# Kernel tuning notes

Measured on AMD Instinct MI355X. Metric: run time of the kernel, lower is better.

The kernel has to match this reference:

```python
import jax, jax.numpy as jnp
import numpy as np

N_NODES = 50000
N_EDGES = 800000
IN_FEAT = 64
HIDDEN = 32
GRID = 4
OUT = 1
N_GRAPHS = 128
N_CONV = 2  # num_layers - 1
NEG_SLOPE = 0.01  # torch LeakyReLU default


def kan_apply(x, W, bias=None):
    # x: (B, in), W: (2, out, in, grid) -> (B, out)
    g = W.shape[-1]
    k = jnp.arange(1, g + 1, dtype=x.dtype)          # (grid,)
    arg = x[:, :, None] * k                           # (B, in, grid)
    y = (jnp.einsum('big,oig->bo', jnp.cos(arg), W[0])
         + jnp.einsum('big,oig->bo', jnp.sin(arg), W[1]))
    if bias is not None:
        y = y + bias
    return y


def setup_inputs() -> dict:
    key = jax.random.key(0)
    ks = jax.random.split(key, 8)
    x = jax.random.normal(ks[0], (N_NODES, IN_FEAT), dtype=jnp.float32)
    edge_index = jax.random.randint(ks[1], (2, N_EDGES), 0, N_NODES, dtype=jnp.int64)
    batch = jnp.sort(jax.random.randint(ks[2], (N_NODES,), 0, N_GRAPHS, dtype=jnp.int64))
    W_in = jax.random.normal(ks[3], (2, HIDDEN, IN_FEAT, GRID), dtype=jnp.float32) / np.float32(np.sqrt(IN_FEAT) * np.sqrt(GRID))
    W_conv = jax.random.normal(ks[4], (N_CONV, 2, HIDDEN, HIDDEN, GRID), dtype=jnp.float32) / np.float32(np.sqrt(HIDDEN) * np.sqrt(GRID))
    W_out = jax.random.normal(ks[5], (2, OUT, HIDDEN, 1), dtype=jnp.float32) / np.float32(np.sqrt(HIDDEN) * 1.0)
    b_out = jnp.zeros((1, OUT), dtype=jnp.float32)
    return {"x": x, "edge_index": edge_index, "batch": batch,
            "W_in": W_in, "W_conv": W_conv, "W_out": W_out, "b_out": b_out}


def reference(x, edge_index, batch, W_in, W_conv, W_out, b_out):
    # input KAN projection: (N, in_feat) -> (N, hidden)
    h = kan_apply(x, W_in)
    src, dst = edge_index[0], edge_index[1]
    for l in range(N_CONV):
        # message: Fourier-KAN transform of gathered source features (E, hidden)
        m_edge = kan_apply(h[src], W_conv[l])
        # aggregate: scatter-add to destination nodes
        m = jax.ops.segment_sum(m_edge, dst, num_segments=N_NODES)
        h = jax.nn.leaky_relu(m + h, negative_slope=NEG_SLOPE)
    # mean pool per graph
    sums = jax.ops.segment_sum(h, batch, num_segments=N_GRAPHS)
    counts = jax.ops.segment_sum(jnp.ones((h.shape[0], 1), h.dtype), batch, num_segments=N_GRAPHS)
    y = sums / jnp.maximum(counts, 1.0)
    # readout: KAN_linear (grid=1, with bias) + sigmoid
    out = jax.nn.sigmoid(kan_apply(y, W_out, b_out))
    return out
```

## Files before the change

### kernel.cpp

```cpp
#include <hip/hip_runtime.h>
#include <math.h>

#define N_NODES   50000
#define N_EDGES   800000
#define IN_FEAT   64
#define HIDDEN    32
#define GRID_SZ   4
#define N_GRAPHS  128
#define NEG_SLOPE 0.01f
#define SCAN_BLOCKS 196
#define NH (N_NODES * HIDDEN)

__global__ __launch_bounds__(256) void zero_int_kernel(int* __restrict__ p, int n) {
  const int i = blockIdx.x * 256 + threadIdx.x;
  if (i < n) p[i] = 0;
}

__global__ __launch_bounds__(256) void hist_kernel(
    const int* __restrict__ dst, int* __restrict__ deg) {
  const int e = blockIdx.x * 256 + threadIdx.x;
  if (e < N_EDGES) atomicAdd(&deg[dst[e]], 1);
}

__global__ __launch_bounds__(256) void scanA_kernel(
    const int* __restrict__ deg, int* __restrict__ bsum) {
  const int i = blockIdx.x * 256 + threadIdx.x;
  int v = (i < N_NODES) ? deg[i] : 0;
#pragma unroll
  for (int o = 32; o > 0; o >>= 1) v += __shfl_down(v, o, 64);
  __shared__ int ws[4];
  if ((threadIdx.x & 63) == 0) ws[threadIdx.x >> 6] = v;
  __syncthreads();
  if (threadIdx.x == 0) bsum[blockIdx.x] = ws[0] + ws[1] + ws[2] + ws[3];
}

__global__ __launch_bounds__(256) void scanB_kernel(
    int* __restrict__ bsum, int* __restrict__ row_ptr,
    float* __restrict__ sums_zero, int nz) {
  __shared__ int sh[256];
  const int t = threadIdx.x;
  int v = (t < SCAN_BLOCKS) ? bsum[t] : 0;
  sh[t] = v;
  __syncthreads();
  for (int o = 1; o < 256; o <<= 1) {
    const int u = (t >= o) ? sh[t - o] : 0;
    __syncthreads();
    sh[t] += u;
    __syncthreads();
  }
  bsum[t] = (t == 0) ? 0 : sh[t - 1];
  if (t == 0) row_ptr[N_NODES] = N_EDGES;
  for (int i = t; i < nz; i += 256) sums_zero[i] = 0.f;
}

__global__ __launch_bounds__(256) void scanC_kernel(
    const int* __restrict__ deg, const int* __restrict__ bsum,
    int* __restrict__ row_ptr, int* __restrict__ cursor) {
  __shared__ int sh[256];
  const int t = threadIdx.x;
  const int i = blockIdx.x * 256 + t;
  const int v = (i < N_NODES) ? deg[i] : 0;
  sh[t] = v;
  __syncthreads();
  for (int o = 1; o < 256; o <<= 1) {
    const int u = (t >= o) ? sh[t - o] : 0;
    __syncthreads();
    sh[t] += u;
    __syncthreads();
  }
  if (i < N_NODES) {
    const int excl = bsum[blockIdx.x] + sh[t] - v;
    row_ptr[i] = excl;
    cursor[i] = excl;
  }
}

__global__ __launch_bounds__(256) void fill_kernel(
    const int* __restrict__ src, const int* __restrict__ dst,
    int* __restrict__ cursor, int* __restrict__ adj) {
  const int e = blockIdx.x * 256 + threadIdx.x;
  if (e < N_EDGES) {
    const int pos = atomicAdd(&cursor[dst[e]], 1);
    adj[pos] = src[e];
  }
}

__global__ __launch_bounds__(256) void gather_update_v3(
    const float* __restrict__ T, const int* __restrict__ row_ptr,
    const int* __restrict__ adj, float* __restrict__ H) {
  const int gid = blockIdx.x * 256 + threadIdx.x;
  const int n = gid >> 3;
  const int q = gid & 7;
  if (n >= N_NODES) return;
  const int lo = row_ptr[n], hi = row_ptr[n + 1];
  const float4* __restrict__ T4 = reinterpret_cast<const float4*>(T);
  float4 acc = make_float4(0.f, 0.f, 0.f, 0.f);
  int k = lo;
  for (; k + 1 < hi; k += 2) {
    const int s0 = adj[k];
    const int s1 = adj[k + 1];
    const float4 t0 = T4[s0 * 8 + q];
    const float4 t1 = T4[s1 * 8 + q];
    acc.x += t0.x + t1.x; acc.y += t0.y + t1.y;
    acc.z += t0.z + t1.z; acc.w += t0.w + t1.w;
  }
  if (k < hi) {
    const float4 t = T4[adj[k] * 8 + q];
    acc.x += t.x; acc.y += t.y; acc.z += t.z; acc.w += t.w;
  }
  float4* __restrict__ H4 = reinterpret_cast<float4*>(H);
  float4 h = H4[n * 8 + q];
  h.x += acc.x; h.y += acc.y; h.z += acc.z; h.w += acc.w;
  h.x = (h.x >= 0.f) ? h.x : NEG_SLOPE * h.x;
  h.y = (h.y >= 0.f) ? h.y : NEG_SLOPE * h.y;
  h.z = (h.z >= 0.f) ? h.z : NEG_SLOPE * h.z;
  h.w = (h.w >= 0.f) ? h.w : NEG_SLOPE * h.w;
  H4[n * 8 + q] = h;
}

__global__ __launch_bounds__(256, 2) void kan_input_v9(
    const float* __restrict__ X, const float* __restrict__ W,
    float* __restrict__ H) {
  extern __shared__ float smem[];
  float4* __restrict__ w4 = reinterpret_cast<float4*>(smem);
  float* __restrict__ tg = smem + 16384;
  const int tid = threadIdx.x;
  const int n0 = blockIdx.x * 128;

  const float4* __restrict__ Wg = reinterpret_cast<const float4*>(W);
#pragma unroll
  for (int r = 0; r < 16; ++r) {
    const int idx = r * 256 + tid;
    const int part = idx >> 11;
    const int rem = idx & 2047;
    const int o = rem >> 6;
    const int i = rem & 63;
    w4[part * 2048 + o * 64 + (i ^ ((o >> 2) & 7))] = Wg[idx];
  }

  const int oq = tid & 7;
  const int grp = tid >> 3;
  const int nb = 4 * grp;

  float acc[4][4];
#pragma unroll
  for (int n = 0; n < 4; ++n)
#pragma unroll
    for (int q = 0; q < 4; ++q) acc[n][q] = 0.f;

  for (int ch = 0; ch < 8; ++ch) {
    __syncthreads();
#pragma unroll
    for (int p = 0; p < 4; ++p) {
      const int lin = p * 256 + tid;
      const int il = lin & 7;
      const int node = lin >> 3;
      const int gn = n0 + node;
      const int gs = (gn < N_NODES) ? gn : (N_NODES - 1);
      const float v = X[gs * IN_FEAT + ch * 8 + il];
      float s1, c1;
      sincosf(v, &s1, &c1);
      *reinterpret_cast<float2*>(&tg[il * 260 + node * 2]) = make_float2(c1, s1);
    }
    __syncthreads();
#pragma unroll
    for (int il = 0; il < 8; ++il) {
      const int i = ch * 8 + il;
      const float4 tA = *reinterpret_cast<const float4*>(&tg[il * 260 + nb * 2]);
      const float4 tB = *reinterpret_cast<const float4*>(&tg[il * 260 + nb * 2 + 4]);
      const float bc[4] = {tA.x, tA.z, tB.x, tB.z};
      const float bs[4] = {tA.y, tA.w, tB.y, tB.w};
      float cN[4][4], sN[4][4];
#pragma unroll
      for (int n = 0; n < 4; ++n) {
        const float c1 = bc[n], s1 = bs[n];
        const float c2 = c1*c1 - s1*s1, s2 = s1*c1 + c1*s1;
        const float c3 = c2*c1 - s2*s1, s3 = s2*c1 + c2*s1;
        const float c4 = c3*c1 - s3*s1, s4 = s3*c1 + c3*s1;
        cN[n][0]=c1; cN[n][1]=c2; cN[n][2]=c3; cN[n][3]=c4;
        sN[n][0]=s1; sN[n][1]=s2; sN[n][2]=s3; sN[n][3]=s4;
      }
      const int sl = i ^ oq;
#pragma unroll
      for (int q = 0; q < 4; ++q) {
        const float4 a = w4[(4 * oq + q) * 64 + sl];
        const float4 b = w4[2048 + (4 * oq + q) * 64 + sl];
#pragma unroll
        for (int n = 0; n < 4; ++n)
          acc[n][q] += cN[n][0]*a.x + cN[n][1]*a.y + cN[n][2]*a.z + cN[n][3]*a.w
                     + sN[n][0]*b.x + sN[n][1]*b.y + sN[n][2]*b.z + sN[n][3]*b.w;
      }
    }
  }
#pragma unroll
  for (int n = 0; n < 4; ++n) {
    const int gn = n0 + nb + n;
    if (gn < N_NODES)
      *reinterpret_cast<float4*>(&H[gn * HIDDEN + 4 * oq]) =
          make_float4(acc[n][0], acc[n][1], acc[n][2], acc[n][3]);
  }
}

__global__ __launch_bounds__(256, 2) void kan_node_v9(
    const float* __restrict__ Hin, const float* __restrict__ W,
    float* __restrict__ T) {
  extern __shared__ float smem[];
  float4* __restrict__ w4 = reinterpret_cast<float4*>(smem);
  float* __restrict__ tg = smem + 8192;
  const int tid = threadIdx.x;
  const int n0 = blockIdx.x * 128;

  const float4* __restrict__ Wg = reinterpret_cast<const float4*>(W);
#pragma unroll
  for (int r = 0; r < 8; ++r) {
    const int idx = r * 256 + tid;
    const int part = idx >> 10;
    const int rem = idx & 1023;
    const int o = rem >> 5;
    const int i = rem & 31;
    w4[part * 1024 + o * 32 + (i ^ ((o >> 2) & 7))] = Wg[idx];
  }

#pragma unroll
  for (int p = 0; p < 16; ++p) {
    const int lin = p * 256 + tid;
    const int il = lin & 31;
    const int node = lin >> 5;
    const int gn = n0 + node;
    const int gs = (gn < N_NODES) ? gn : (N_NODES - 1);
    const float v = Hin[gs * HIDDEN + il];
    float s1, c1;
    sincosf(v, &s1, &c1);
    *reinterpret_cast<float2*>(&tg[il * 260 + node * 2]) = make_float2(c1, s1);
  }
  __syncthreads();

  const int oq = tid & 7;
  const int grp = tid >> 3;
  const int nb = 4 * grp;

  float acc[4][4];
#pragma unroll
  for (int n = 0; n < 4; ++n)
#pragma unroll
    for (int q = 0; q < 4; ++q) acc[n][q] = 0.f;

#pragma unroll 4
  for (int i = 0; i < HIDDEN; ++i) {
    const float4 tA = *reinterpret_cast<const float4*>(&tg[i * 260 + nb * 2]);
    const float4 tB = *reinterpret_cast<const float4*>(&tg[i * 260 + nb * 2 + 4]);
    const float bc[4] = {tA.x, tA.z, tB.x, tB.z};
    const float bs[4] = {tA.y, tA.w, tB.y, tB.w};
    float cN[4][4], sN[4][4];
#pragma unroll
    for (int n = 0; n < 4; ++n) {
      const float c1 = bc[n], s1 = bs[n];
      const float c2 = c1*c1 - s1*s1, s2 = s1*c1 + c1*s1;
      const float c3 = c2*c1 - s2*s1, s3 = s2*c1 + c2*s1;
      const float c4 = c3*c1 - s3*s1, s4 = s3*c1 + c3*s1;
      cN[n][0]=c1; cN[n][1]=c2; cN[n][2]=c3; cN[n][3]=c4;
      sN[n][0]=s1; sN[n][1]=s2; sN[n][2]=s3; sN[n][3]=s4;
    }
    const int sl = i ^ oq;
#pragma unroll
    for (int q = 0; q < 4; ++q) {
      const float4 a = w4[(4 * oq + q) * 32 + sl];
      const float4 b = w4[1024 + (4 * oq + q) * 32 + sl];
#pragma unroll
      for (int n = 0; n < 4; ++n)
        acc[n][q] += cN[n][0]*a.x + cN[n][1]*a.y + cN[n][2]*a.z + cN[n][3]*a.w
                   + sN[n][0]*b.x + sN[n][1]*b.y + sN[n][2]*b.z + sN[n][3]*b.w;
    }
  }
#pragma unroll
  for (int n = 0; n < 4; ++n) {
    const int gn = n0 + nb + n;
    if (gn < N_NODES)
      *reinterpret_cast<float4*>(&T[gn * HIDDEN + 4 * oq]) =
          make_float4(acc[n][0], acc[n][1], acc[n][2], acc[n][3]);
  }
}

#define POOL_RANGES 2048
__global__ __launch_bounds__(256) void pool_rl(
    const float* __restrict__ H, const int* __restrict__ batch,
    float* __restrict__ sums, float* __restrict__ cnt) {
  const int tid = threadIdx.x;
  const int f = tid & 31;
  const int r = blockIdx.x * 8 + (tid >> 5);
  const int PER = (N_NODES + POOL_RANGES - 1) / POOL_RANGES;
  int n = r * PER;
  const int end = (n + PER < N_NODES) ? n + PER : N_NODES;
  if (n >= end) return;
  int g = batch[n];
  float acc = 0.f, c = 0.f;
  for (; n < end; ++n) {
    const int gn = batch[n];
    if (gn != g) {
      atomicAdd(&sums[g * HIDDEN + f], acc);
      if (f == 0) atomicAdd(&cnt[g], c);
      g = gn; acc = 0.f; c = 0.f;
    }
    acc += H[n * HIDDEN + f];
    c += 1.f;
  }
  atomicAdd(&sums[g * HIDDEN + f], acc);
  if (f == 0) atomicAdd(&cnt[g], c);
}

__global__ __launch_bounds__(128) void readout_kernel(
    const float* __restrict__ sums, const float* __restrict__ cnt,
    const float* __restrict__ Wout, const float* __restrict__ bout,
    float* __restrict__ out) {
  const int g = threadIdx.x;
  if (g < N_GRAPHS) {
    const float c = fmaxf(cnt[g], 1.0f);
    float z = 0.f;
#pragma unroll
    for (int i = 0; i < HIDDEN; ++i) {
      const float y = sums[g * HIDDEN + i] / c;
      z += cosf(y) * Wout[i] + sinf(y) * Wout[HIDDEN + i];
    }
    z += bout[0];
    out[g] = 1.0f / (1.0f + expf(-z));
  }
}

extern "C" void kernel_launch(void* const* d_in, const int* in_sizes, int n_in,
                              void* d_out, int out_size, void* d_ws, size_t ws_size,
                              hipStream_t stream) {
  const float* x        = (const float*)d_in[0];
  const int*   eidx     = (const int*)d_in[1];
  const int*   batch    = (const int*)d_in[2];
  const float* W_in     = (const float*)d_in[3];
  const float* W_conv   = (const float*)d_in[4];
  const float* W_out    = (const float*)d_in[5];
  const float* b_out    = (const float*)d_in[6];
  float* out            = (float*)d_out;

  const int* src = eidx;
  const int* dst = eidx + N_EDGES;

  float* ws = (float*)d_ws;
  float* H       = ws;
  float* T       = ws + NH;
  int*   row_ptr = (int*)(ws + 2 * NH);
  int*   deg     = row_ptr + 50008;
  int*   cursor  = deg + 50048;
  int*   bsum    = cursor + 50048;
  int*   adj     = bsum + 256;
  float* SUMS    = (float*)(adj + 800000);
  float* CNT     = SUMS + 4096;

  const int kan_blocks  = (N_NODES + 127) / 128;
  const int edge_blocks = (N_EDGES + 255) / 256;
  const int gath_blocks = (N_NODES * 8 + 255) / 256;

  const size_t in_lds   = (size_t)(16384 + 8 * 260) * 4;
  const size_t conv_lds = (size_t)(8192 + 32 * 260) * 4;
  const int WCONV_STRIDE = 2 * HIDDEN * HIDDEN * GRID_SZ;

  zero_int_kernel<<<SCAN_BLOCKS, 256, 0, stream>>>(deg, N_NODES);
  hist_kernel<<<edge_blocks, 256, 0, stream>>>(dst, deg);
  scanA_kernel<<<SCAN_BLOCKS, 256, 0, stream>>>(deg, bsum);
  scanB_kernel<<<1, 256, 0, stream>>>(bsum, row_ptr, SUMS, N_GRAPHS * HIDDEN + N_GRAPHS);
  scanC_kernel<<<SCAN_BLOCKS, 256, 0, stream>>>(deg, bsum, row_ptr, cursor);
  fill_kernel<<<edge_blocks, 256, 0, stream>>>(src, dst, cursor, adj);

  kan_input_v9<<<kan_blocks, 256, in_lds, stream>>>(x, W_in, H);

  kan_node_v9<<<kan_blocks, 256, conv_lds, stream>>>(H, W_conv, T);
  gather_update_v3<<<gath_blocks, 256, 0, stream>>>(T, row_ptr, adj, H);

  kan_node_v9<<<kan_blocks, 256, conv_lds, stream>>>(H, W_conv + WCONV_STRIDE, T);
  gather_update_v3<<<gath_blocks, 256, 0, stream>>>(T, row_ptr, adj, H);

  pool_rl<<<POOL_RANGES / 8, 256, 0, stream>>>(H, batch, SUMS, CNT);
  readout_kernel<<<1, 128, 0, stream>>>(SUMS, CNT, W_out, b_out, out);
}
```

Baseline: 273.8 us.

## Read KAN weights directly from global/L1 instead of staging them in LDS

```diff
diff --git a/kernel.cpp b/kernel.cpp
--- a/kernel.cpp
+++ b/kernel.cpp
@@ -118,137 +118,47 @@
   H4[n * 8 + q] = h;
 }
 
-__global__ __launch_bounds__(256, 2) void kan_input_v9(
+__global__ __launch_bounds__(256, 2) void kan_input_v13(
     const float* __restrict__ X, const float* __restrict__ W,
     float* __restrict__ H) {
-  extern __shared__ float smem[];
-  float4* __restrict__ w4 = reinterpret_cast<float4*>(smem);
-  float* __restrict__ tg = smem + 16384;
+  extern __shared__ float tg[];
   const int tid = threadIdx.x;
   const int n0 = blockIdx.x * 128;
 
-  const float4* __restrict__ Wg = reinterpret_cast<const float4*>(W);
-#pragma unroll
-  for (int r = 0; r < 16; ++r) {
-    const int idx = r * 256 + tid;
-    const int part = idx >> 11;
-    const int rem = idx & 2047;
-    const int o = rem >> 6;
-    const int i = rem & 63;
-    w4[part * 2048 + o * 64 + (i ^ ((o >> 2) & 7))] = Wg[idx];
-  }
+  {
+    const int i = tid & 63;
+    const int w = tid >> 6;
+#pragma unroll
+    for (int p = 0; p < 32; ++p) {
+      const int node = p * 4 + w;
+      const int gn = n0 + node;
+      const int gs = (gn < N_NODES) ? gn : (N_NODES - 1);
+      const float v = X[gs * IN_FEAT + i];
+      float s1, c1;
+      sincosf(v, &s1, &c1);
+      *reinterpret_cast<float2*>(&tg[i * 257 + node * 2]) = make_float2(c1, s1);
+    }
+  }
+  __syncthreads();
 
   const int oq = tid & 7;
   const int grp = tid >> 3;
   const int nb = 4 * grp;
 
+  const float4* __restrict__ Wg = reinterpret_cast<const float4*>(W);
+  const float4* __restrict__ WC = Wg + (4 * oq) * 64;
+  const float4* __restrict__ WS = Wg + 2048 + (4 * oq) * 64;
+
   float acc[4][4];
 #pragma unroll
   for (int n = 0; n < 4; ++n)
 #pragma unroll
     for (int q = 0; q < 4; ++q) acc[n][q] = 0.f;
 
-  for (int ch = 0; ch < 8; ++ch) {
-    __syncthreads();
-#pragma unroll
-    for (int p = 0; p < 4; ++p) {
-      const int lin = p * 256 + tid;
-      const int il = lin & 7;
-      const int node = lin >> 3;
-      const int gn = n0 + node;
-      const int gs = (gn < N_NODES) ? gn : (N_NODES - 1);
-      const float v = X[gs * IN_FEAT + ch * 8 + il];
-      float s1, c1;
-      sincosf(v, &s1, &c1);
-      *reinterpret_cast<float2*>(&tg[il * 260 + node * 2]) = make_float2(c1, s1);
-    }
-    __syncthreads();
-#pragma unroll
-    for (int il = 0; il < 8; ++il) {
-      const int i = ch * 8 + il;
-      const float4 tA = *reinterpret_cast<const float4*>(&tg[il * 260 + nb * 2]);
-      const float4 tB = *reinterpret_cast<const float4*>(&tg[il * 260 + nb * 2 + 4]);
-      const float bc[4] = {tA.x, tA.z, tB.x, tB.z};
-      const float bs[4] = {tA.y, tA.w, tB.y, tB.w};
-      float cN[4][4], sN[4][4];
-#pragma unroll
-      for (int n = 0; n < 4; ++n) {
-        const float c1 = bc[n], s1 = bs[n];
-        const float c2 = c1*c1 - s1*s1, s2 = s1*c1 + c1*s1;
-        const float c3 = c2*c1 - s2*s1, s3 = s2*c1 + c2*s1;
-        const float c4 = c3*c1 - s3*s1, s4 = s3*c1 + c3*s1;
-        cN[n][0]=c1; cN[n][1]=c2; cN[n][2]=c3; cN[n][3]=c4;
-        sN[n][0]=s1; sN[n][1]=s2; sN[n][2]=s3; sN[n][3]=s4;
-      }
-      const int sl = i ^ oq;
-#pragma unroll
-      for (int q = 0; q < 4; ++q) {
-        const float4 a = w4[(4 * oq + q) * 64 + sl];
-        const float4 b = w4[2048 + (4 * oq + q) * 64 + sl];
-#pragma unroll
-        for (int n = 0; n < 4; ++n)
-          acc[n][q] += cN[n][0]*a.x + cN[n][1]*a.y + cN[n][2]*a.z + cN[n][3]*a.w
-                     + sN[n][0]*b.x + sN[n][1]*b.y + sN[n][2]*b.z + sN[n][3]*b.w;
-      }
-    }
-  }
-#pragma unroll
-  for (int n = 0; n < 4; ++n) {
-    const int gn = n0 + nb + n;
-    if (gn < N_NODES)
-      *reinterpret_cast<float4*>(&H[gn * HIDDEN + 4 * oq]) =
-          make_float4(acc[n][0], acc[n][1], acc[n][2], acc[n][3]);
-  }
-}
-
-__global__ __launch_bounds__(256, 2) void kan_node_v9(
-    const float* __restrict__ Hin, const float* __restrict__ W,
-    float* __restrict__ T) {
-  extern __shared__ float smem[];
-  float4* __restrict__ w4 = reinterpret_cast<float4*>(smem);
-  float* __restrict__ tg = smem + 8192;
-  const int tid = threadIdx.x;
-  const int n0 = blockIdx.x * 128;
-
-  const float4* __restrict__ Wg = reinterpret_cast<const float4*>(W);
-#pragma unroll
-  for (int r = 0; r < 8; ++r) {
-    const int idx = r * 256 + tid;
-    const int part = idx >> 10;
-    const int rem = idx & 1023;
-    const int o = rem >> 5;
-    const int i = rem & 31;
-    w4[part * 1024 + o * 32 + (i ^ ((o >> 2) & 7))] = Wg[idx];
-  }
-
-#pragma unroll
-  for (int p = 0; p < 16; ++p) {
-    const int lin = p * 256 + tid;
-    const int il = lin & 31;
-    const int node = lin >> 5;
-    const int gn = n0 + node;
-    const int gs = (gn < N_NODES) ? gn : (N_NODES - 1);
-    const float v = Hin[gs * HIDDEN + il];
-    float s1, c1;
-    sincosf(v, &s1, &c1);
-    *reinterpret_cast<float2*>(&tg[il * 260 + node * 2]) = make_float2(c1, s1);
-  }
-  __syncthreads();
-
-  const int oq = tid & 7;
-  const int grp = tid >> 3;
-  const int nb = 4 * grp;
-
-  float acc[4][4];
-#pragma unroll
-  for (int n = 0; n < 4; ++n)
-#pragma unroll
-    for (int q = 0; q < 4; ++q) acc[n][q] = 0.f;
-
 #pragma unroll 4
-  for (int i = 0; i < HIDDEN; ++i) {
-    const float4 tA = *reinterpret_cast<const float4*>(&tg[i * 260 + nb * 2]);
-    const float4 tB = *reinterpret_cast<const float4*>(&tg[i * 260 + nb * 2 + 4]);
+  for (int i = 0; i < IN_FEAT; ++i) {
+    const float4 tA = *reinterpret_cast<const float4*>(&tg[i * 257 + nb * 2]);
+    const float4 tB = *reinterpret_cast<const float4*>(&tg[i * 257 + nb * 2 + 4]);
     const float bc[4] = {tA.x, tA.z, tB.x, tB.z};
     const float bs[4] = {tA.y, tA.w, tB.y, tB.w};
     float cN[4][4], sN[4][4];
@@ -261,11 +171,82 @@
       cN[n][0]=c1; cN[n][1]=c2; cN[n][2]=c3; cN[n][3]=c4;
       sN[n][0]=s1; sN[n][1]=s2; sN[n][2]=s3; sN[n][3]=s4;
     }
-    const int sl = i ^ oq;
 #pragma unroll
     for (int q = 0; q < 4; ++q) {
-      const float4 a = w4[(4 * oq + q) * 32 + sl];
-      const float4 b = w4[1024 + (4 * oq + q) * 32 + sl];
+      const float4 a = WC[q * 64 + i];
+      const float4 b = WS[q * 64 + i];
+#pragma unroll
+      for (int n = 0; n < 4; ++n)
+        acc[n][q] += cN[n][0]*a.x + cN[n][1]*a.y + cN[n][2]*a.z + cN[n][3]*a.w
+                   + sN[n][0]*b.x + sN[n][1]*b.y + sN[n][2]*b.z + sN[n][3]*b.w;
+    }
+  }
+#pragma unroll
+  for (int n = 0; n < 4; ++n) {
+    const int gn = n0 + nb + n;
+    if (gn < N_NODES)
+      *reinterpret_cast<float4*>(&H[gn * HIDDEN + 4 * oq]) =
+          make_float4(acc[n][0], acc[n][1], acc[n][2], acc[n][3]);
+  }
+}
+
+__global__ __launch_bounds__(256, 3) void kan_node_v13(
+    const float* __restrict__ Hin, const float* __restrict__ W,
+    float* __restrict__ T) {
+  extern __shared__ float tg[];
+  const int tid = threadIdx.x;
+  const int n0 = blockIdx.x * 128;
+
+  {
+    const int i = tid & 31;
+    const int hw = tid >> 5;
+#pragma unroll
+    for (int p = 0; p < 16; ++p) {
+      const int node = p * 8 + hw;
+      const int gn = n0 + node;
+      const int gs = (gn < N_NODES) ? gn : (N_NODES - 1);
+      const float v = Hin[gs * HIDDEN + i];
+      float s1, c1;
+      sincosf(v, &s1, &c1);
+      *reinterpret_cast<float2*>(&tg[i * 257 + node * 2]) = make_float2(c1, s1);
+    }
+  }
+  __syncthreads();
+
+  const int oq = tid & 7;
+  const int grp = tid >> 3;
+  const int nb = 4 * grp;
+
+  const float4* __restrict__ Wg = reinterpret_cast<const float4*>(W);
+  const float4* __restrict__ WC = Wg + (4 * oq) * 32;
+  const float4* __restrict__ WS = Wg + 1024 + (4 * oq) * 32;
+
+  float acc[4][4];
+#pragma unroll
+  for (int n = 0; n < 4; ++n)
+#pragma unroll
+    for (int q = 0; q < 4; ++q) acc[n][q] = 0.f;
+
+#pragma unroll 4
+  for (int i = 0; i < HIDDEN; ++i) {
+    const float4 tA = *reinterpret_cast<const float4*>(&tg[i * 257 + nb * 2]);
+    const float4 tB = *reinterpret_cast<const float4*>(&tg[i * 257 + nb * 2 + 4]);
+    const float bc[4] = {tA.x, tA.z, tB.x, tB.z};
+    const float bs[4] = {tA.y, tA.w, tB.y, tB.w};
+    float cN[4][4], sN[4][4];
+#pragma unroll
+    for (int n = 0; n < 4; ++n) {
+      const float c1 = bc[n], s1 = bs[n];
+      const float c2 = c1*c1 - s1*s1, s2 = s1*c1 + c1*s1;
+      const float c3 = c2*c1 - s2*s1, s3 = s2*c1 + c2*s1;
+      const float c4 = c3*c1 - s3*s1, s4 = s3*c1 + c3*s1;
+      cN[n][0]=c1; cN[n][1]=c2; cN[n][2]=c3; cN[n][3]=c4;
+      sN[n][0]=s1; sN[n][1]=s2; sN[n][2]=s3; sN[n][3]=s4;
+    }
+#pragma unroll
+    for (int q = 0; q < 4; ++q) {
+      const float4 a = WC[q * 32 + i];
+      const float4 b = WS[q * 32 + i];
 #pragma unroll
       for (int n = 0; n < 4; ++n)
         acc[n][q] += cN[n][0]*a.x + cN[n][1]*a.y + cN[n][2]*a.z + cN[n][3]*a.w
@@ -356,8 +337,8 @@
   const int edge_blocks = (N_EDGES + 255) / 256;
   const int gath_blocks = (N_NODES * 8 + 255) / 256;
 
-  const size_t in_lds   = (size_t)(16384 + 8 * 260) * 4;
-  const size_t conv_lds = (size_t)(8192 + 32 * 260) * 4;
+  const size_t in_lds   = (size_t)(64 * 257) * 4;
+  const size_t conv_lds = (size_t)(32 * 257) * 4;
   const int WCONV_STRIDE = 2 * HIDDEN * HIDDEN * GRID_SZ;
 
   zero_int_kernel<<<SCAN_BLOCKS, 256, 0, stream>>>(deg, N_NODES);
@@ -367,12 +348,12 @@
   scanC_kernel<<<SCAN_BLOCKS, 256, 0, stream>>>(deg, bsum, row_ptr, cursor);
   fill_kernel<<<edge_blocks, 256, 0, stream>>>(src, dst, cursor, adj);
 
-  kan_input_v9<<<kan_blocks, 256, in_lds, stream>>>(x, W_in, H);
-
-  kan_node_v9<<<kan_blocks, 256, conv_lds, stream>>>(H, W_conv, T);
+  kan_input_v13<<<kan_blocks, 256, in_lds, stream>>>(x, W_in, H);
+
+  kan_node_v13<<<kan_blocks, 256, conv_lds, stream>>>(H, W_conv, T);
   gather_update_v3<<<gath_blocks, 256, 0, stream>>>(T, row_ptr, adj, H);
 
-  kan_node_v9<<<kan_blocks, 256, conv_lds, stream>>>(H, W_conv + WCONV_STRIDE, T);
+  kan_node_v13<<<kan_blocks, 256, conv_lds, stream>>>(H, W_conv + WCONV_STRIDE, T);
   gather_update_v3<<<gath_blocks, 256, 0, stream>>>(T, row_ptr, adj, H);
 
   pool_rl<<<POOL_RANGES / 8, 256, 0, stream>>>(H, batch, SUMS, CNT);
```

Result: slower. 485.5 us (+77.3%).
